# Kernel optimization log

Hardware: AMD Instinct MI355X
Metric: run time of the kernel (lower is better)

The kernel has to match this reference:

```python
import jax, jax.numpy as jnp
import numpy as np

B, M = 512, 32          # graphs, atoms per graph
N = B * M               # 16384 nodes
F_IN, H, L = 16, 128, 2 # input feat, hidden, n interaction layers
CUTOFF = 1.0
BOX = 2.0               # side of position box -> avg degree ~16 at r=1


def _glorot(k, shape):
    fan_in = shape[-2]
    return jax.random.normal(k, shape, dtype=jnp.float32) / np.sqrt(fan_in)


def setup_inputs():
    key = jax.random.key(0)
    ks = jax.random.split(key, 12)
    return {
        "h": jax.random.normal(ks[0], (N, F_IN), dtype=jnp.float32),
        "x": jax.random.uniform(ks[1], (N, 3), dtype=jnp.float32) * BOX,
        "batch": jnp.repeat(jnp.arange(B, dtype=jnp.int32), M),
        "W_in": _glorot(ks[2], (F_IN, H)), "b_in": jnp.zeros((H,), jnp.float32),
        "We1": _glorot(ks[3], (L, 2 * H + 1, H)), "be1": jnp.zeros((L, H), jnp.float32),
        "We2": _glorot(ks[4], (L, H, H)), "be2": jnp.zeros((L, H), jnp.float32),
        "Wh1": _glorot(ks[5], (L, 2 * H, H)), "bh1": jnp.zeros((L, H), jnp.float32),
        "Wh2": _glorot(ks[6], (L, H, H)), "bh2": jnp.zeros((L, H), jnp.float32),
        "W_out": _glorot(ks[7], (H, H)), "b_out": jnp.zeros((H,), jnp.float32),
        "Wn1": _glorot(ks[8], (H, H)), "bn1": jnp.zeros((H,), jnp.float32),
        "Wn2": _glorot(ks[9], (H, 1)), "bn2": jnp.zeros((1,), jnp.float32),
    }


def reference(h, x, batch, W_in, b_in, We1, be1, We2, be2, Wh1, bh1, Wh2, bh2, W_out, b_out, Wn1, bn1, Wn2, bn2):
    # radius graph within each molecule, fixed-shape dense mask [B,M,M]
    xg = x.reshape(B, M, 3)
    diff = xg[:, :, None, :] - xg[:, None, :, :]                 # [B,M,M,3]
    d2 = jnp.sum(diff * diff, axis=-1)                            # [B,M,M]
    adj = (d2 < CUTOFF * CUTOFF) & (~jnp.eye(M, dtype=bool))      # no self-loops

    hg = (h @ W_in + b_in).reshape(B, M, H)                       # embedding_in
    for l in range(L):  # sake_conv interaction layers
        Wa, Wb, wd = We1[l, :H], We1[l, H:2 * H], We1[l, 2 * H]
        mi = jnp.einsum('bmh,hk->bmk', hg, Wa)
        mj = jnp.einsum('bmh,hk->bmk', hg, Wb)
        # edge message phi_e([h_i, h_j, ||x_i-x_j||^2])
        m = jax.nn.silu(mi[:, :, None, :] + mj[:, None, :, :] + d2[..., None] * wd + be1[l])
        m = jax.nn.silu(jnp.einsum('bijh,hk->bijk', m, We2[l]) + be2[l])
        m = jnp.where(adj[..., None], m, 0.0)
        agg = jnp.sum(m, axis=2)                                  # scatter-add over neighbors j
        # node update phi_h([h_i, m_i]) with residual
        u = jax.nn.silu(jnp.einsum('bmh,hk->bmk', hg, Wh1[l, :H])
                        + jnp.einsum('bmh,hk->bmk', agg, Wh1[l, H:]) + bh1[l])
        hg = hg + jnp.einsum('bmh,hk->bmk', u, Wh2[l]) + bh2[l]

    ho = hg.reshape(N, H) @ W_out + b_out                         # embedding_out
    e = jax.nn.silu(ho @ Wn1 + bn1) @ Wn2 + bn2                   # energy_network -> [N,1]
    out = jax.ops.segment_sum(e, batch, num_segments=B)           # per-graph energy pooling
    return out.squeeze()
```

## Files before the change

kernel.cpp:

```cpp
#include <hip/hip_runtime.h>
#include <hip/hip_bf16.h>


#define NB 512

typedef __bf16 bf16x8 __attribute__((ext_vector_type(8)));
typedef __bf16 bf16x2 __attribute__((ext_vector_type(2)));
typedef float f32x4 __attribute__((ext_vector_type(4)));

__device__ __forceinline__ unsigned short f2bf(float f) {
    unsigned int u = __float_as_uint(f);
    u = u + 0x7FFFu + ((u >> 16) & 1u);
    return (unsigned short)(u >> 16);
}
__device__ __forceinline__ unsigned int packbf(float lo, float hi) {
    bf16x2 t;
    t.x = (__bf16)lo;
    t.y = (__bf16)hi;
    return __builtin_bit_cast(unsigned int, t);
}
__device__ __forceinline__ float bflo(unsigned int u) { return __uint_as_float(u << 16); }
__device__ __forceinline__ float bfhi(unsigned int u) { return __uint_as_float(u & 0xffff0000u); }
__device__ __forceinline__ float silu_f(float v) {
    return v * __builtin_amdgcn_rcpf(1.0f + __expf(-v));
}

__global__ __launch_bounds__(256) void prep_weights(
        const float* __restrict__ We1, const float* __restrict__ We2,
        const float* __restrict__ Wh1, const float* __restrict__ Wh2,
        const float* __restrict__ W_out, const float* __restrict__ Wn1,
        unsigned short* __restrict__ ws) {
    __shared__ unsigned short t[32][33];
    const int mtx  = blockIdx.x >> 4;
    const int tile = blockIdx.x & 15;
    const int kt = tile >> 2, nt = tile & 3;
    const int tx = threadIdx.x & 31, ty = threadIdx.x >> 5;

    const int l    = (mtx < 12) ? (mtx / 6) : 0;
    const int kind = (mtx < 12) ? (mtx % 6) : (6 + (mtx - 12));
    const float* src = nullptr;
    switch (kind) {
        case 0: src = We1 + (size_t)(l*257      )*128; break;
        case 1: src = We1 + (size_t)(l*257 + 128)*128; break;
        case 2: src = We2 + (size_t)(l*128      )*128; break;
        case 3: src = Wh1 + (size_t)(l*256      )*128; break;
        case 4: src = Wh1 + (size_t)(l*256 + 128)*128; break;
        case 5: src = Wh2 + (size_t)(l*128      )*128; break;
        case 6: src = W_out; break;
        case 7: src = Wn1;  break;
    }
    #pragma unroll
    for (int r = 0; r < 4; r++) {
        int k = kt*32 + ty + r*8;
        int n = nt*32 + tx;
        t[tx][ty + r*8] = f2bf(src[(size_t)k*128 + n]);
    }
    __syncthreads();
    unsigned short* dst = ws + ((size_t)mtx << 14);
    #pragma unroll
    for (int r = 0; r < 4; r++) {
        int nl = ty + r*8;
        int n = nt*32 + nl, k = kt*32 + tx;
        dst[(size_t)n*128 + k] = t[nl][tx];
    }
}

#define MFMA16(ACC, A, B) (ACC) = __builtin_amdgcn_mfma_f32_16x16x32_bf16((A), (B), (ACC), 0, 0, 0)

__global__ __launch_bounds__(256, 2) void sake_kernel(
    const float* __restrict__ h,   const float* __restrict__ x,
    const float* __restrict__ W_in,const float* __restrict__ b_in,
    const float* __restrict__ We1, const float* __restrict__ be1,
    const float* __restrict__ be2, const float* __restrict__ bh1,
    const float* __restrict__ bh2, const float* __restrict__ b_out,
    const float* __restrict__ bn1, const float* __restrict__ Wn2,
    const float* __restrict__ bn2, const unsigned short* __restrict__ wt,
    float* __restrict__ out)
{
    __shared__ __align__(16) float          s_d2[32*32];
    __shared__ __align__(16) float          s_hg[32*129];
    __shared__ __align__(16) unsigned short s_mimj[32*264];
    __shared__ __align__(16) unsigned short s_A1[32*136];
    __shared__ __align__(16) unsigned short s_A2[32*136];
    __shared__ __align__(16) float          s_wd[128];
    __shared__ __align__(16) float          s_be2[128];
    __shared__ __align__(16) float          s_x[32*4];
    __shared__ __align__(16) float          s_ep[256];
    __shared__ unsigned char s_nbr[32][16];
    __shared__ int           s_cnt[32];

    const int tid  = threadIdx.x;
    const int b    = blockIdx.x;
    const int w    = tid >> 6;
    const int lane = tid & 63;
    const int quad = lane >> 4;
    const int lm   = lane & 15;
    const int mt   = w & 1;
    const int ng   = w >> 1;

    if (tid < 32) {
        s_x[tid*4+0] = x[(b*32+tid)*3+0];
        s_x[tid*4+1] = x[(b*32+tid)*3+1];
        s_x[tid*4+2] = x[(b*32+tid)*3+2];
    }
    __syncthreads();
    for (int p = tid; p < 1024; p += 256) {
        int i = p >> 5, j = p & 31;
        float dx = s_x[i*4+0]-s_x[j*4+0];
        float dy = s_x[i*4+1]-s_x[j*4+1];
        float dz = s_x[i*4+2]-s_x[j*4+2];
        s_d2[p] = dx*dx + dy*dy + dz*dz;
    }
    {
        int k = tid & 127, mg = tid >> 7;
        float c0 = W_in[       k], c1 = W_in[ 128+k], c2 = W_in[ 256+k], c3 = W_in[ 384+k];
        float c4 = W_in[ 512+k], c5 = W_in[ 640+k], c6 = W_in[ 768+k], c7 = W_in[ 896+k];
        float c8 = W_in[1024+k], c9 = W_in[1152+k], c10= W_in[1280+k], c11= W_in[1408+k];
        float c12= W_in[1536+k], c13= W_in[1664+k], c14= W_in[1792+k], c15= W_in[1920+k];
        float bi = b_in[k];
        for (int rr = 0; rr < 16; rr++) {
            int m = mg*16 + rr;
            const float4* h4 = (const float4*)(h + (size_t)(b*32 + m)*16);
            float4 h0 = h4[0], h1 = h4[1], h2 = h4[2], h3 = h4[3];
            float acc = bi
                + h0.x*c0  + h0.y*c1  + h0.z*c2  + h0.w*c3
                + h1.x*c4  + h1.y*c5  + h1.z*c6  + h1.w*c7
                + h2.x*c8  + h2.y*c9  + h2.z*c10 + h2.w*c11
                + h3.x*c12 + h3.y*c13 + h3.z*c14 + h3.w*c15;
            s_hg[m*129 + k] = acc;
        }
    }
    __syncthreads();

    if (tid < 32) {
        int c = 0;
        for (int j = 0; j < 32; j++) {
            if (s_d2[tid*32 + j] < 1.0f && j != tid) {
                if (c < 16) s_nbr[tid][c] = (unsigned char)j;
                c++;
            }
        }
        for (int q = c; q < 16; q++) s_nbr[tid][q] = (unsigned char)tid;
        s_cnt[tid] = c;
    }

    for (int l = 0; l < 2; l++) {
        {
            int m = tid >> 3, c = (tid & 7) * 16;
            const float* hp = &s_hg[m*129 + c];
            uint4 pa, pb;
            pa.x = packbf(hp[0],  hp[1]);  pa.y = packbf(hp[2],  hp[3]);
            pa.z = packbf(hp[4],  hp[5]);  pa.w = packbf(hp[6],  hp[7]);
            pb.x = packbf(hp[8],  hp[9]);  pb.y = packbf(hp[10], hp[11]);
            pb.z = packbf(hp[12], hp[13]); pb.w = packbf(hp[14], hp[15]);
            *(uint4*)&s_A1[m*136 + c]     = pa;
            *(uint4*)&s_A1[m*136 + c + 8] = pb;
        }
        if (tid < 128) {
            s_wd[tid]  = We1[(l*257 + 256)*128 + tid];
            s_be2[tid] = be2[l*128 + tid];
        }
        __syncthreads();

        #pragma unroll 1
        for (int t4 = 0; t4 < 8; t4++) {
            int nt = ng + t4*2;
            const unsigned short* bt = wt + (((size_t)l*6 + (nt < 8 ? 0 : 1)) << 14);
            int ncl = (nt & 7)*16 + lm;
            f32x4 acc = {0.f,0.f,0.f,0.f};
            #pragma unroll
            for (int kb = 0; kb < 4; kb++) {
                bf16x8 a  = *(const bf16x8*)&s_A1[(mt*16+lm)*136 + kb*32 + quad*8];
                bf16x8 bb = *(const bf16x8*)&bt[ncl*128 + kb*32 + quad*8];
                MFMA16(acc, a, bb);
            }
            int c = nt*16 + lm;
            float bias = (nt >= 8) ? be1[l*128 + ncl] : 0.0f;
            s_mimj[(mt*16 + quad*4 + 0)*264 + c] = f2bf(acc.x + bias);
            s_mimj[(mt*16 + quad*4 + 1)*264 + c] = f2bf(acc.y + bias);
            s_mimj[(mt*16 + quad*4 + 2)*264 + c] = f2bf(acc.z + bias);
            s_mimj[(mt*16 + quad*4 + 3)*264 + c] = f2bf(acc.w + bias);
        }
        __syncthreads();

        {
            const unsigned short* we2t = wt + (((size_t)l*6 + 2) << 14);
            const unsigned short* bbase = we2t + lm*128 + quad*8;
            bf16x8 b0 = *(const bf16x8*)(bbase      );
            bf16x8 b1 = *(const bf16x8*)(bbase +  32);
            bf16x8 b2 = *(const bf16x8*)(bbase +  64);
            bf16x8 b3 = *(const bf16x8*)(bbase +  96);
            #pragma unroll 1
            for (int ii = 0; ii < 8; ii++) {
                const int i = ii*4 + w;
                const int cnt = s_cnt[i];
                const uint4 miu0 = *(const uint4*)&s_mimj[i*264 +  0 + quad*8];
                const uint4 miu1 = *(const uint4*)&s_mimj[i*264 + 32 + quad*8];
                const uint4 miu2 = *(const uint4*)&s_mimj[i*264 + 64 + quad*8];
                const uint4 miu3 = *(const uint4*)&s_mimj[i*264 + 96 + quad*8];
#define MAKE_AF(J, KB, MIU, AF) { \
    const uint4 mju = *(const uint4*)&s_mimj[(J)*264 + 128 + (KB)*32 + quad*8]; \
    const float4 wa = *(const float4*)&s_wd[(KB)*32 + quad*8]; \
    const float4 wb = *(const float4*)&s_wd[(KB)*32 + quad*8 + 4]; \
    uint4 au; \
    au.x = packbf(silu_f(bflo(MIU.x)+bflo(mju.x)+d2v*wa.x), silu_f(bfhi(MIU.x)+bfhi(mju.x)+d2v*wa.y)); \
    au.y = packbf(silu_f(bflo(MIU.y)+bflo(mju.y)+d2v*wa.z), silu_f(bfhi(MIU.y)+bfhi(mju.y)+d2v*wa.w)); \
    au.z = packbf(silu_f(bflo(MIU.z)+bflo(mju.z)+d2v*wb.x), silu_f(bfhi(MIU.z)+bfhi(mju.z)+d2v*wb.y)); \
    au.w = packbf(silu_f(bflo(MIU.w)+bflo(mju.w)+d2v*wb.z), silu_f(bfhi(MIU.w)+bfhi(mju.w)+d2v*wb.w)); \
    AF = __builtin_bit_cast(bf16x8, au); }
                if (cnt <= 16) {
                    const int j = s_nbr[i][lm];
                    const float d2v = s_d2[i*32 + j];
                    bf16x8 a00, a01, a02, a03;
                    MAKE_AF(j, 0, miu0, a00) MAKE_AF(j, 1, miu1, a01)
                    MAKE_AF(j, 2, miu2, a02) MAKE_AF(j, 3, miu3, a03)
                    const int jb0 = quad*4;
                    const float mk00 = (jb0 + 0 < cnt) ? 1.f : 0.f;
                    const float mk01 = (jb0 + 1 < cnt) ? 1.f : 0.f;
                    const float mk02 = (jb0 + 2 < cnt) ? 1.f : 0.f;
                    const float mk03 = (jb0 + 3 < cnt) ? 1.f : 0.f;
                    #pragma unroll 1
                    for (int nt = 0; nt < 8; nt++) {
                        const unsigned short* np = bbase + (((nt + 1) & 7) * 2048);
                        bf16x8 n0 = *(const bf16x8*)(np      );
                        bf16x8 n1 = *(const bf16x8*)(np +  32);
                        bf16x8 n2 = *(const bf16x8*)(np +  64);
                        bf16x8 n3 = *(const bf16x8*)(np +  96);
                        f32x4 ac0 = {0.f,0.f,0.f,0.f};
                        MFMA16(ac0, a00, b0); MFMA16(ac0, a01, b1);
                        MFMA16(ac0, a02, b2); MFMA16(ac0, a03, b3);
                        const float bv = s_be2[nt*16 + lm];
                        float part = mk00*silu_f(ac0.x + bv) + mk01*silu_f(ac0.y + bv)
                                   + mk02*silu_f(ac0.z + bv) + mk03*silu_f(ac0.w + bv);
                        part += __shfl_xor(part, 16);
                        part += __shfl_xor(part, 32);
                        if (lane < 16) s_A2[i*136 + nt*16 + lane] = f2bf(part);
                        b0 = n0; b1 = n1; b2 = n2; b3 = n3;
                    }
                } else {
                    bf16x8 a00, a01, a02, a03;
                    bf16x8 a10, a11, a12, a13;
                    {
                        const int j = lm;
                        const float d2v = s_d2[i*32 + j];
                        MAKE_AF(j, 0, miu0, a00) MAKE_AF(j, 1, miu1, a01)
                        MAKE_AF(j, 2, miu2, a02) MAKE_AF(j, 3, miu3, a03)
                    }
                    {
                        const int j = 16 + lm;
                        const float d2v = s_d2[i*32 + j];
                        MAKE_AF(j, 0, miu0, a10) MAKE_AF(j, 1, miu1, a11)
                        MAKE_AF(j, 2, miu2, a12) MAKE_AF(j, 3, miu3, a13)
                    }
                    const int jb0 = quad*4, jb1 = 16 + quad*4;
                    const float mk00 = (s_d2[i*32 + jb0 + 0] < 1.0f && (jb0+0) != i) ? 1.f : 0.f;
                    const float mk01 = (s_d2[i*32 + jb0 + 1] < 1.0f && (jb0+1) != i) ? 1.f : 0.f;
                    const float mk02 = (s_d2[i*32 + jb0 + 2] < 1.0f && (jb0+2) != i) ? 1.f : 0.f;
                    const float mk03 = (s_d2[i*32 + jb0 + 3] < 1.0f && (jb0+3) != i) ? 1.f : 0.f;
                    const float mk10 = (s_d2[i*32 + jb1 + 0] < 1.0f && (jb1+0) != i) ? 1.f : 0.f;
                    const float mk11 = (s_d2[i*32 + jb1 + 1] < 1.0f && (jb1+1) != i) ? 1.f : 0.f;
                    const float mk12 = (s_d2[i*32 + jb1 + 2] < 1.0f && (jb1+2) != i) ? 1.f : 0.f;
                    const float mk13 = (s_d2[i*32 + jb1 + 3] < 1.0f && (jb1+3) != i) ? 1.f : 0.f;
                    #pragma unroll 1
                    for (int nt = 0; nt < 8; nt++) {
                        const unsigned short* np = bbase + (((nt + 1) & 7) * 2048);
                        bf16x8 n0 = *(const bf16x8*)(np      );
                        bf16x8 n1 = *(const bf16x8*)(np +  32);
                        bf16x8 n2 = *(const bf16x8*)(np +  64);
                        bf16x8 n3 = *(const bf16x8*)(np +  96);
                        f32x4 ac0 = {0.f,0.f,0.f,0.f};
                        f32x4 ac1 = {0.f,0.f,0.f,0.f};
                        MFMA16(ac0, a00, b0); MFMA16(ac0, a01, b1);
                        MFMA16(ac0, a02, b2); MFMA16(ac0, a03, b3);
                        MFMA16(ac1, a10, b0); MFMA16(ac1, a11, b1);
                        MFMA16(ac1, a12, b2); MFMA16(ac1, a13, b3);
                        const float bv = s_be2[nt*16 + lm];
                        float part = mk00*silu_f(ac0.x + bv) + mk01*silu_f(ac0.y + bv)
                                   + mk02*silu_f(ac0.z + bv) + mk03*silu_f(ac0.w + bv)
                                   + mk10*silu_f(ac1.x + bv) + mk11*silu_f(ac1.y + bv)
                                   + mk12*silu_f(ac1.z + bv) + mk13*silu_f(ac1.w + bv);
                        part += __shfl_xor(part, 16);
                        part += __shfl_xor(part, 32);
                        if (lane < 16) s_A2[i*136 + nt*16 + lane] = f2bf(part);
                        b0 = n0; b1 = n1; b2 = n2; b3 = n3;
                    }
                }
#undef MAKE_AF
            }
        }
        __syncthreads();

        unsigned short* s_u = s_mimj;
        {
            const unsigned short* w1a = wt + (((size_t)l*6 + 3) << 14);
            const unsigned short* w1b = wt + (((size_t)l*6 + 4) << 14);
#define U_GEMM(T2) { \
    const int nt = ng + (T2)*2, ncl = nt*16 + lm; \
    f32x4 acc = {0.f,0.f,0.f,0.f}; \
    _Pragma("unroll") \
    for (int kb = 0; kb < 4; kb++) { \
        bf16x8 a  = *(const bf16x8*)&s_A1[(mt*16+lm)*136 + kb*32 + quad*8]; \
        bf16x8 bb = *(const bf16x8*)&w1a[ncl*128 + kb*32 + quad*8]; \
        MFMA16(acc, a, bb); } \
    _Pragma("unroll") \
    for (int kb = 0; kb < 4; kb++) { \
        bf16x8 a  = *(const bf16x8*)&s_A2[(mt*16+lm)*136 + kb*32 + quad*8]; \
        bf16x8 bb = *(const bf16x8*)&w1b[ncl*128 + kb*32 + quad*8]; \
        MFMA16(acc, a, bb); } \
    const float bh = bh1[l*128 + ncl]; \
    s_u[(mt*16 + quad*4 + 0)*136 + ncl] = f2bf(silu_f(acc.x + bh)); \
    s_u[(mt*16 + quad*4 + 1)*136 + ncl] = f2bf(silu_f(acc.y + bh)); \
    s_u[(mt*16 + quad*4 + 2)*136 + ncl] = f2bf(silu_f(acc.z + bh)); \
    s_u[(mt*16 + quad*4 + 3)*136 + ncl] = f2bf(silu_f(acc.w + bh)); }
            U_GEMM(0) U_GEMM(1) U_GEMM(2) U_GEMM(3)
#undef U_GEMM
        }
        __syncthreads();

        {
            const unsigned short* w2 = wt + (((size_t)l*6 + 5) << 14);
#define H_GEMM(T2) { \
    const int nt = ng + (T2)*2, ncl = nt*16 + lm; \
    f32x4 acc = {0.f,0.f,0.f,0.f}; \
    _Pragma("unroll") \
    for (int kb = 0; kb < 4; kb++) { \
        bf16x8 a  = *(const bf16x8*)&s_u[(mt*16+lm)*136 + kb*32 + quad*8]; \
        bf16x8 bb = *(const bf16x8*)&w2[ncl*128 + kb*32 + quad*8]; \
        MFMA16(acc, a, bb); } \
    const float bh = bh2[l*128 + ncl]; \
    s_hg[(mt*16 + quad*4 + 0)*129 + ncl] += acc.x + bh; \
    s_hg[(mt*16 + quad*4 + 1)*129 + ncl] += acc.y + bh; \
    s_hg[(mt*16 + quad*4 + 2)*129 + ncl] += acc.z + bh; \
    s_hg[(mt*16 + quad*4 + 3)*129 + ncl] += acc.w + bh; }
            H_GEMM(0) H_GEMM(1) H_GEMM(2) H_GEMM(3)
#undef H_GEMM
        }
        __syncthreads();
    }

    {
        int m = tid >> 3, c = (tid & 7) * 16;
        const float* hp = &s_hg[m*129 + c];
        uint4 pa, pb;
        pa.x = packbf(hp[0],  hp[1]);  pa.y = packbf(hp[2],  hp[3]);
        pa.z = packbf(hp[4],  hp[5]);  pa.w = packbf(hp[6],  hp[7]);
        pb.x = packbf(hp[8],  hp[9]);  pb.y = packbf(hp[10], hp[11]);
        pb.z = packbf(hp[12], hp[13]); pb.w = packbf(hp[14], hp[15]);
        *(uint4*)&s_A1[m*136 + c]     = pa;
        *(uint4*)&s_A1[m*136 + c + 8] = pb;
    }
    __syncthreads();
    {
        const unsigned short* wo = wt + ((size_t)12 << 14);
#define O_GEMM(T2) { \
    const int nt = ng + (T2)*2, ncl = nt*16 + lm; \
    f32x4 acc = {0.f,0.f,0.f,0.f}; \
    _Pragma("unroll") \
    for (int kb = 0; kb < 4; kb++) { \
        bf16x8 a  = *(const bf16x8*)&s_A1[(mt*16+lm)*136 + kb*32 + quad*8]; \
        bf16x8 bb = *(const bf16x8*)&wo[ncl*128 + kb*32 + quad*8]; \
        MFMA16(acc, a, bb); } \
    const float bo = b_out[ncl]; \
    s_A2[(mt*16 + quad*4 + 0)*136 + ncl] = f2bf(acc.x + bo); \
    s_A2[(mt*16 + quad*4 + 1)*136 + ncl] = f2bf(acc.y + bo); \
    s_A2[(mt*16 + quad*4 + 2)*136 + ncl] = f2bf(acc.z + bo); \
    s_A2[(mt*16 + quad*4 + 3)*136 + ncl] = f2bf(acc.w + bo); }
        O_GEMM(0) O_GEMM(1) O_GEMM(2) O_GEMM(3)
#undef O_GEMM
    }
    __syncthreads();
    float* s_g = (float*)s_mimj;
    {
        const unsigned short* wn1 = wt + ((size_t)13 << 14);
#define G_GEMM(T2) { \
    const int nt = ng + (T2)*2, ncl = nt*16 + lm; \
    f32x4 acc = {0.f,0.f,0.f,0.f}; \
    _Pragma("unroll") \
    for (int kb = 0; kb < 4; kb++) { \
        bf16x8 a  = *(const bf16x8*)&s_A2[(mt*16+lm)*136 + kb*32 + quad*8]; \
        bf16x8 bb = *(const bf16x8*)&wn1[ncl*128 + kb*32 + quad*8]; \
        MFMA16(acc, a, bb); } \
    const float bn = bn1[ncl]; \
    s_g[(mt*16 + quad*4 + 0)*129 + ncl] = silu_f(acc.x + bn); \
    s_g[(mt*16 + quad*4 + 1)*129 + ncl] = silu_f(acc.y + bn); \
    s_g[(mt*16 + quad*4 + 2)*129 + ncl] = silu_f(acc.z + bn); \
    s_g[(mt*16 + quad*4 + 3)*129 + ncl] = silu_f(acc.w + bn); }
        G_GEMM(0) G_GEMM(1) G_GEMM(2) G_GEMM(3)
#undef G_GEMM
    }
    __syncthreads();
    {
        int m = tid >> 3, s = tid & 7;
        float acc = 0.f;
        #pragma unroll
        for (int q = 0; q < 16; q++) {
            int hh = s*16 + q;
            acc += s_g[m*129 + hh] * Wn2[hh];
        }
        s_ep[tid] = acc;
    }
    __syncthreads();
    if (tid < 32) {
        float e = bn2[0];
        #pragma unroll
        for (int s = 0; s < 8; s++) e += s_ep[tid*8 + s];
        #pragma unroll
        for (int off = 16; off >= 1; off >>= 1) e += __shfl_down(e, off, 32);
        if (tid == 0) out[b] = e;
    }
}

extern "C" void kernel_launch(void* const* d_in, const int* in_sizes, int n_in,
                              void* d_out, int out_size, void* d_ws, size_t ws_size,
                              hipStream_t stream) {
    const float* h     = (const float*)d_in[0];
    const float* x     = (const float*)d_in[1];
    const float* W_in  = (const float*)d_in[3];
    const float* b_in  = (const float*)d_in[4];
    const float* We1   = (const float*)d_in[5];
    const float* be1   = (const float*)d_in[6];
    const float* We2   = (const float*)d_in[7];
    const float* be2   = (const float*)d_in[8];
    const float* Wh1   = (const float*)d_in[9];
    const float* bh1   = (const float*)d_in[10];
    const float* Wh2   = (const float*)d_in[11];
    const float* bh2   = (const float*)d_in[12];
    const float* W_out = (const float*)d_in[13];
    const float* b_out = (const float*)d_in[14];
    const float* Wn1   = (const float*)d_in[15];
    const float* bn1   = (const float*)d_in[16];
    const float* Wn2   = (const float*)d_in[17];
    const float* bn2   = (const float*)d_in[18];
    unsigned short* ws = (unsigned short*)d_ws;
    float* outp = (float*)d_out;

    prep_weights<<<14*16, 256, 0, stream>>>(We1, We2, Wh1, Wh2, W_out, Wn1, ws);
    sake_kernel<<<NB, 256, 0, stream>>>(h, x, W_in, b_in, We1, be1, be2, bh1, bh2,
                                        b_out, bn1, Wn2, bn2, ws, outp);
}
```

Before: 257.8 us.

## Shrink shared memory to fit three blocks per CU, compact neighbor distances

Drops the dense 32x32 distance table, the staged positions and the energy-partial buffer from shared memory. Neighbor lists and their squared distances are now built with wave shuffles into a compact 32x16 array, and s_ep reuses that array. The rare dense fallback recomputes distances from global x and builds masks with ballots. Launch bounds go from 2 to 3 blocks per CU, which trades register budget for occupancy, and be2 is now stored as bf16, which slightly changes its precision.

```diff
diff --git a/kernel.cpp b/kernel.cpp
--- a/kernel.cpp
+++ b/kernel.cpp
@@ -21,6 +21,7 @@
 }
 __device__ __forceinline__ float bflo(unsigned int u) { return __uint_as_float(u << 16); }
 __device__ __forceinline__ float bfhi(unsigned int u) { return __uint_as_float(u & 0xffff0000u); }
+__device__ __forceinline__ float bf2f(unsigned short u) { return __uint_as_float((unsigned int)u << 16); }
 __device__ __forceinline__ float silu_f(float v) {
     return v * __builtin_amdgcn_rcpf(1.0f + __expf(-v));
 }
@@ -67,7 +68,7 @@
 
 #define MFMA16(ACC, A, B) (ACC) = __builtin_amdgcn_mfma_f32_16x16x32_bf16((A), (B), (ACC), 0, 0, 0)
 
-__global__ __launch_bounds__(256, 2) void sake_kernel(
+__global__ __launch_bounds__(256, 3) void sake_kernel(
     const float* __restrict__ h,   const float* __restrict__ x,
     const float* __restrict__ W_in,const float* __restrict__ b_in,
     const float* __restrict__ We1, const float* __restrict__ be1,
@@ -77,17 +78,15 @@
     const float* __restrict__ bn2, const unsigned short* __restrict__ wt,
     float* __restrict__ out)
 {
-    __shared__ __align__(16) float          s_d2[32*32];
     __shared__ __align__(16) float          s_hg[32*129];
     __shared__ __align__(16) unsigned short s_mimj[32*264];
     __shared__ __align__(16) unsigned short s_A1[32*136];
     __shared__ __align__(16) unsigned short s_A2[32*136];
+    __shared__ __align__(16) float          s_nd2[32*16];
     __shared__ __align__(16) float          s_wd[128];
-    __shared__ __align__(16) float          s_be2[128];
-    __shared__ __align__(16) float          s_x[32*4];
-    __shared__ __align__(16) float          s_ep[256];
-    __shared__ unsigned char s_nbr[32][16];
-    __shared__ int           s_cnt[32];
+    __shared__ __align__(16) unsigned short s_be2[128];
+    __shared__ __align__(16) unsigned char  s_nbr[32][16];
+    __shared__ __align__(16) unsigned char  s_cnt[32];
 
     const int tid  = threadIdx.x;
     const int b    = blockIdx.x;
@@ -99,17 +98,23 @@
     const int ng   = w >> 1;
 
     if (tid < 32) {
-        s_x[tid*4+0] = x[(b*32+tid)*3+0];
-        s_x[tid*4+1] = x[(b*32+tid)*3+1];
-        s_x[tid*4+2] = x[(b*32+tid)*3+2];
-    }
-    __syncthreads();
-    for (int p = tid; p < 1024; p += 256) {
-        int i = p >> 5, j = p & 31;
-        float dx = s_x[i*4+0]-s_x[j*4+0];
-        float dy = s_x[i*4+1]-s_x[j*4+1];
-        float dz = s_x[i*4+2]-s_x[j*4+2];
-        s_d2[p] = dx*dx + dy*dy + dz*dz;
+        const float xx = x[(b*32+tid)*3+0];
+        const float xy = x[(b*32+tid)*3+1];
+        const float xz = x[(b*32+tid)*3+2];
+        int c = 0;
+        for (int j = 0; j < 32; j++) {
+            float ox = __shfl(xx, j);
+            float oy = __shfl(xy, j);
+            float oz = __shfl(xz, j);
+            float dx = xx - ox, dy = xy - oy, dz = xz - oz;
+            float d2 = dx*dx + dy*dy + dz*dz;
+            if (d2 < 1.0f && j != tid) {
+                if (c < 16) { s_nbr[tid][c] = (unsigned char)j; s_nd2[tid*16 + c] = d2; }
+                c++;
+            }
+        }
+        for (int q = c; q < 16; q++) { s_nbr[tid][q] = (unsigned char)tid; s_nd2[tid*16 + q] = 0.0f; }
+        s_cnt[tid] = (unsigned char)c;
     }
     {
         int k = tid & 127, mg = tid >> 7;
@@ -132,18 +137,6 @@
     }
     __syncthreads();
 
-    if (tid < 32) {
-        int c = 0;
-        for (int j = 0; j < 32; j++) {
-            if (s_d2[tid*32 + j] < 1.0f && j != tid) {
-                if (c < 16) s_nbr[tid][c] = (unsigned char)j;
-                c++;
-            }
-        }
-        for (int q = c; q < 16; q++) s_nbr[tid][q] = (unsigned char)tid;
-        s_cnt[tid] = c;
-    }
-
     for (int l = 0; l < 2; l++) {
         {
             int m = tid >> 3, c = (tid & 7) * 16;
@@ -158,7 +151,7 @@
         }
         if (tid < 128) {
             s_wd[tid]  = We1[(l*257 + 256)*128 + tid];
-            s_be2[tid] = be2[l*128 + tid];
+            s_be2[tid] = f2bf(be2[l*128 + tid]);
         }
         __syncthreads();
 
@@ -210,7 +203,7 @@
     AF = __builtin_bit_cast(bf16x8, au); }
                 if (cnt <= 16) {
                     const int j = s_nbr[i][lm];
-                    const float d2v = s_d2[i*32 + j];
+                    const float d2v = s_nd2[i*16 + lm];
                     bf16x8 a00, a01, a02, a03;
                     MAKE_AF(j, 0, miu0, a00) MAKE_AF(j, 1, miu1, a01)
                     MAKE_AF(j, 2, miu2, a02) MAKE_AF(j, 3, miu3, a03)
@@ -229,7 +222,7 @@
                         f32x4 ac0 = {0.f,0.f,0.f,0.f};
                         MFMA16(ac0, a00, b0); MFMA16(ac0, a01, b1);
                         MFMA16(ac0, a02, b2); MFMA16(ac0, a03, b3);
-                        const float bv = s_be2[nt*16 + lm];
+                        const float bv = bf2f(s_be2[nt*16 + lm]);
                         float part = mk00*silu_f(ac0.x + bv) + mk01*silu_f(ac0.y + bv)
                                    + mk02*silu_f(ac0.z + bv) + mk03*silu_f(ac0.w + bv);
                         part += __shfl_xor(part, 16);
@@ -238,29 +231,42 @@
                         b0 = n0; b1 = n1; b2 = n2; b3 = n3;
                     }
                 } else {
+                    const float xi0 = x[(b*32+i)*3+0];
+                    const float xi1 = x[(b*32+i)*3+1];
+                    const float xi2 = x[(b*32+i)*3+2];
+                    float da0 = xi0 - x[(b*32+lm)*3+0];
+                    float da1 = xi1 - x[(b*32+lm)*3+1];
+                    float da2 = xi2 - x[(b*32+lm)*3+2];
+                    const float d2a = da0*da0 + da1*da1 + da2*da2;
+                    float db0 = xi0 - x[(b*32+16+lm)*3+0];
+                    float db1 = xi1 - x[(b*32+16+lm)*3+1];
+                    float db2 = xi2 - x[(b*32+16+lm)*3+2];
+                    const float d2b = db0*db0 + db1*db1 + db2*db2;
+                    const unsigned long long balA = __ballot(d2a < 1.0f && lm != i);
+                    const unsigned long long balB = __ballot(d2b < 1.0f && (16+lm) != i);
                     bf16x8 a00, a01, a02, a03;
                     bf16x8 a10, a11, a12, a13;
                     {
                         const int j = lm;
-                        const float d2v = s_d2[i*32 + j];
+                        const float d2v = d2a;
                         MAKE_AF(j, 0, miu0, a00) MAKE_AF(j, 1, miu1, a01)
                         MAKE_AF(j, 2, miu2, a02) MAKE_AF(j, 3, miu3, a03)
                     }
                     {
                         const int j = 16 + lm;
-                        const float d2v = s_d2[i*32 + j];
+                        const float d2v = d2b;
                         MAKE_AF(j, 0, miu0, a10) MAKE_AF(j, 1, miu1, a11)
                         MAKE_AF(j, 2, miu2, a12) MAKE_AF(j, 3, miu3, a13)
                     }
-                    const int jb0 = quad*4, jb1 = 16 + quad*4;
-                    const float mk00 = (s_d2[i*32 + jb0 + 0] < 1.0f && (jb0+0) != i) ? 1.f : 0.f;
-                    const float mk01 = (s_d2[i*32 + jb0 + 1] < 1.0f && (jb0+1) != i) ? 1.f : 0.f;
-                    const float mk02 = (s_d2[i*32 + jb0 + 2] < 1.0f && (jb0+2) != i) ? 1.f : 0.f;
-                    const float mk03 = (s_d2[i*32 + jb0 + 3] < 1.0f && (jb0+3) != i) ? 1.f : 0.f;
-                    const float mk10 = (s_d2[i*32 + jb1 + 0] < 1.0f && (jb1+0) != i) ? 1.f : 0.f;
-                    const float mk11 = (s_d2[i*32 + jb1 + 1] < 1.0f && (jb1+1) != i) ? 1.f : 0.f;
-                    const float mk12 = (s_d2[i*32 + jb1 + 2] < 1.0f && (jb1+2) != i) ? 1.f : 0.f;
-                    const float mk13 = (s_d2[i*32 + jb1 + 3] < 1.0f && (jb1+3) != i) ? 1.f : 0.f;
+                    const int jb0 = quad*4;
+                    const float mk00 = ((balA >> (jb0 + 0)) & 1ull) ? 1.f : 0.f;
+                    const float mk01 = ((balA >> (jb0 + 1)) & 1ull) ? 1.f : 0.f;
+                    const float mk02 = ((balA >> (jb0 + 2)) & 1ull) ? 1.f : 0.f;
+                    const float mk03 = ((balA >> (jb0 + 3)) & 1ull) ? 1.f : 0.f;
+                    const float mk10 = ((balB >> (jb0 + 0)) & 1ull) ? 1.f : 0.f;
+                    const float mk11 = ((balB >> (jb0 + 1)) & 1ull) ? 1.f : 0.f;
+                    const float mk12 = ((balB >> (jb0 + 2)) & 1ull) ? 1.f : 0.f;
+                    const float mk13 = ((balB >> (jb0 + 3)) & 1ull) ? 1.f : 0.f;
                     #pragma unroll 1
                     for (int nt = 0; nt < 8; nt++) {
                         const unsigned short* np = bbase + (((nt + 1) & 7) * 2048);
@@ -274,7 +280,7 @@
                         MFMA16(ac0, a02, b2); MFMA16(ac0, a03, b3);
                         MFMA16(ac1, a10, b0); MFMA16(ac1, a11, b1);
                         MFMA16(ac1, a12, b2); MFMA16(ac1, a13, b3);
-                        const float bv = s_be2[nt*16 + lm];
+                        const float bv = bf2f(s_be2[nt*16 + lm]);
                         float part = mk00*silu_f(ac0.x + bv) + mk01*silu_f(ac0.y + bv)
                                    + mk02*silu_f(ac0.z + bv) + mk03*silu_f(ac0.w + bv)
                                    + mk10*silu_f(ac1.x + bv) + mk11*silu_f(ac1.y + bv)
@@ -389,6 +395,7 @@
 #undef G_GEMM
     }
     __syncthreads();
+    float* s_ep = s_nd2;
     {
         int m = tid >> 3, s = tid & 7;
         float acc = 0.f;
```

Result: slower. 263.7 us (+2.3%).
